# Kernel optimization log

Hardware: AMD Instinct MI355X
Metric: run time of the kernel (lower is better)

## Reference

```python
import jax, jax.numpy as jnp
import numpy as np
import math

B, N, DIM = 16, 1024, 384
DEPTH, HEADS, DH = 6, 6, 64
INNER = HEADS * DH          # 384
MLP = 1536
LN_EPS = 1e-5


def setup_inputs() -> dict:
    key = jax.random.key(0)
    ks = jax.random.split(key, 7)
    s = 0.02
    x = jax.random.normal(ks[0], (B, N, DIM), dtype=jnp.float32)
    ln1_g = jnp.ones((DEPTH, DIM), jnp.float32)
    ln1_b = jnp.zeros((DEPTH, DIM), jnp.float32)
    qkv_w = jax.random.normal(ks[1], (DEPTH, DIM, 3 * INNER), jnp.float32) * s
    temp = jnp.full((DEPTH,), math.log(DH ** -0.5), jnp.float32)
    out_w = jax.random.normal(ks[2], (DEPTH, INNER, DIM), jnp.float32) * s
    out_b = jnp.zeros((DEPTH, DIM), jnp.float32)
    ln2_g = jnp.ones((DEPTH, DIM), jnp.float32)
    ln2_b = jnp.zeros((DEPTH, DIM), jnp.float32)
    ff_w1 = jax.random.normal(ks[3], (DEPTH, DIM, MLP), jnp.float32) * s
    ff_b1 = jnp.zeros((DEPTH, MLP), jnp.float32)
    ff_w2 = jax.random.normal(ks[4], (DEPTH, MLP, DIM), jnp.float32) * s
    ff_b2 = jnp.zeros((DEPTH, DIM), jnp.float32)
    return dict(x=x, ln1_g=ln1_g, ln1_b=ln1_b, qkv_w=qkv_w, temp=temp,
                out_w=out_w, out_b=out_b, ln2_g=ln2_g, ln2_b=ln2_b,
                ff_w1=ff_w1, ff_b1=ff_b1, ff_w2=ff_w2, ff_b2=ff_b2)


def _ln(x, g, b):
    m = jnp.mean(x, axis=-1, keepdims=True)
    v = jnp.var(x, axis=-1, keepdims=True)
    return (x - m) * jax.lax.rsqrt(v + LN_EPS) * g + b


def reference(x, ln1_g, ln1_b, qkv_w, temp, out_w, out_b,
              ln2_g, ln2_b, ff_w1, ff_b1, ff_w2, ff_b2):
    neg = -jnp.finfo(x.dtype).max
    eye = jnp.eye(N, dtype=bool)

    def step(x, p):
        g1, b1, wqkv, t, wo, bo, g2, b2, w1, bb1, w2, bb2 = p
        # --- PreNorm + LSA attention ---
        h = _ln(x, g1, b1)
        qkv = h @ wqkv                              # [B, N, 3*INNER]
        q, k, v = jnp.split(qkv, 3, axis=-1)
        split_heads = lambda a: a.reshape(B, N, HEADS, DH).transpose(0, 2, 1, 3)
        q, k, v = split_heads(q), split_heads(k), split_heads(v)
        dots = jnp.einsum('bhnd,bhmd->bhnm', q, k) * jnp.exp(t)
        dots = jnp.where(eye, neg, dots)            # mask diagonal (LSA)
        attn = jax.nn.softmax(dots, axis=-1)
        o = jnp.einsum('bhnm,bhmd->bhnd', attn, v)
        o = o.transpose(0, 2, 1, 3).reshape(B, N, INNER)
        x = x + o @ wo + bo
        # --- PreNorm + FeedForward (exact GELU) ---
        h2 = _ln(x, g2, b2)
        ff = jax.nn.gelu(h2 @ w1 + bb1, approximate=False) @ w2 + bb2
        x = x + ff
        return x, None

    params = (ln1_g, ln1_b, qkv_w, temp, out_w, out_b,
              ln2_g, ln2_b, ff_w1, ff_b1, ff_w2, ff_b2)
    x, _ = jax.lax.scan(step, x, params)
    return x
```

## Files before the change

### kernel.cpp

```cpp
#include <hip/hip_runtime.h>
#include <hip/hip_bf16.h>
#include <math.h>

#define B_     16
#define NTOK   1024
#define DIM_   384
#define DEPTH_ 6
#define HEADS_ 6
#define DH_    64
#define MLP_   1536
#define MTOT   (B_ * NTOK)
#define NBH    (B_ * HEADS_)
#define QKV_PLANE ((size_t)NBH * NTOK * DH_)

typedef unsigned short u16;
typedef unsigned int u32;
typedef short short8 __attribute__((ext_vector_type(8)));
typedef float f32x4 __attribute__((ext_vector_type(4)));

static __device__ __forceinline__ u16 f2b(float f) {
    __hip_bfloat16 h = __float2bfloat16(f);
    return *reinterpret_cast<u16*>(&h);
}

#define GLOAD_LDS16(gp, lp)                                                     \
    __builtin_amdgcn_global_load_lds(                                           \
        (const __attribute__((address_space(1))) void*)(gp),                    \
        (__attribute__((address_space(3))) void*)(lp), 16, 0, 0)

#define WAIT_VM(N)                                                              \
    do { asm volatile("s_waitcnt vmcnt(" #N ")" ::: "memory");                  \
         __builtin_amdgcn_sched_barrier(0); } while (0)
#define WAIT_LGKM0()                                                            \
    do { asm volatile("s_waitcnt lgkmcnt(0)" ::: "memory");                     \
         __builtin_amdgcn_sched_barrier(0); } while (0)

__launch_bounds__(256)
__global__ void transpose_w_kernel(const float* __restrict__ W, u16* __restrict__ WT,
                                   int K, int N) {
    const int layer = blockIdx.z;
    W  += (size_t)layer * K * N;
    WT += (size_t)layer * K * N;
    __shared__ u16 tile[64 * 72];
    const int t = threadIdx.x;
    const int k0 = blockIdx.x * 64, n0 = blockIdx.y * 64;
    const int row = t >> 2, cs = (t & 3) * 16;
    const float4* src = reinterpret_cast<const float4*>(W + (size_t)(k0 + row) * N + n0 + cs);
#pragma unroll
    for (int i = 0; i < 4; i++) {
        float4 f = src[i];
        tile[row * 72 + cs + i * 4 + 0] = f2b(f.x);
        tile[row * 72 + cs + i * 4 + 1] = f2b(f.y);
        tile[row * 72 + cs + i * 4 + 2] = f2b(f.z);
        tile[row * 72 + cs + i * 4 + 3] = f2b(f.w);
    }
    __syncthreads();
    const int nrow = row, ks = cs;
    u16 vals[16] __attribute__((aligned(16)));
#pragma unroll
    for (int e = 0; e < 16; e++) vals[e] = tile[(ks + e) * 72 + nrow];
    u16* dst = WT + (size_t)(n0 + nrow) * K + k0 + ks;
    *reinterpret_cast<short8*>(dst)     = *reinterpret_cast<short8*>(&vals[0]);
    *reinterpret_cast<short8*>(dst + 8) = *reinterpret_cast<short8*>(&vals[8]);
}

__launch_bounds__(256)
__global__ void ln_kernel(const float* __restrict__ x, const float* __restrict__ g,
                          const float* __restrict__ b, u16* __restrict__ h) {
    const int tok  = blockIdx.x * 4 + (threadIdx.x >> 6);
    const int lane = threadIdx.x & 63;
    const float* xr = x + (size_t)tok * DIM_;
    float v[6];
    float s = 0.f;
#pragma unroll
    for (int i = 0; i < 6; i++) { v[i] = xr[lane + i * 64]; s += v[i]; }
#pragma unroll
    for (int m = 1; m < 64; m <<= 1) s += __shfl_xor(s, m);
    const float mean = s * (1.f / 384.f);
    float qs = 0.f;
#pragma unroll
    for (int i = 0; i < 6; i++) { float d = v[i] - mean; qs += d * d; }
#pragma unroll
    for (int m = 1; m < 64; m <<= 1) qs += __shfl_xor(qs, m);
    const float inv = rsqrtf(qs * (1.f / 384.f) + 1e-5f);
    u16* hr = h + (size_t)tok * DIM_;
#pragma unroll
    for (int i = 0; i < 6; i++) {
        const int c = lane + i * 64;
        hr[c] = f2b((v[i] - mean) * inv * g[c] + b[c]);
    }
}

enum { EPI_QKV = 0, EPI_RES = 1, EPI_GELU = 2 };

template <int EPI>
__launch_bounds__(256)
__global__ void gemm_kernel(const u16* __restrict__ A, const u16* __restrict__ BT, int K,
                            const float* __restrict__ bias, const float* __restrict__ resid,
                            float* __restrict__ outf, u16* __restrict__ outb, int ldc,
                            u16* __restrict__ qkv_base) {
    __shared__ u16 As[3][4096];
    __shared__ u16 Bs[3][4096];
    const int t = threadIdx.x;
    const int lane = t & 63, w = t >> 6;
    const int wm = w >> 1, wn = w & 1;
    const int m0 = blockIdx.x * 128, n0 = blockIdx.y * 128;

    f32x4 acc[4][4] = {};

    const int c0p = w * 1024, c1p = w * 1024 + 512;
    const int seg = (lane & 3) * 8;
    const u16* agp0 = A  + (size_t)(m0 + (w * 2 + 0) * 16 + (lane >> 2)) * K + seg;
    const u16* agp1 = A  + (size_t)(m0 + (w * 2 + 1) * 16 + (lane >> 2)) * K + seg;
    const u16* bgp0 = BT + (size_t)(n0 + (w * 2 + 0) * 16 + (lane >> 2)) * K + seg;
    const u16* bgp1 = BT + (size_t)(n0 + (w * 2 + 1) * 16 + (lane >> 2)) * K + seg;

    const int T = K >> 5;
    GLOAD_LDS16(agp0,      &As[0][c0p]);
    GLOAD_LDS16(agp1,      &As[0][c1p]);
    GLOAD_LDS16(bgp0,      &Bs[0][c0p]);
    GLOAD_LDS16(bgp1,      &Bs[0][c1p]);
    GLOAD_LDS16(agp0 + 32, &As[1][c0p]);
    GLOAD_LDS16(agp1 + 32, &As[1][c1p]);
    GLOAD_LDS16(bgp0 + 32, &Bs[1][c0p]);
    GLOAD_LDS16(bgp1 + 32, &Bs[1][c1p]);

    int b0 = 0, b1 = 1, b2 = 2;
    for (int tt = 0; tt < T; ++tt) {
        if (tt + 2 < T) {
            const int kk = (tt + 2) << 5;
            GLOAD_LDS16(agp0 + kk, &As[b2][c0p]);
            GLOAD_LDS16(agp1 + kk, &As[b2][c1p]);
            GLOAD_LDS16(bgp0 + kk, &Bs[b2][c0p]);
            GLOAD_LDS16(bgp1 + kk, &Bs[b2][c1p]);
            WAIT_VM(8);
        } else if (tt + 1 < T) {
            WAIT_VM(4);
        } else {
            WAIT_VM(0);
        }
        __builtin_amdgcn_s_barrier();
        short8 af[4], bf[4];
#pragma unroll
        for (int i = 0; i < 4; i++)
            af[i] = *reinterpret_cast<const short8*>(
                &As[b0][(wm * 64 + i * 16 + (lane & 15)) * 32 + (lane >> 4) * 8]);
#pragma unroll
        for (int j = 0; j < 4; j++)
            bf[j] = *reinterpret_cast<const short8*>(
                &Bs[b0][(wn * 64 + j * 16 + (lane & 15)) * 32 + (lane >> 4) * 8]);
#pragma unroll
        for (int i = 0; i < 4; i++)
#pragma unroll
            for (int j = 0; j < 4; j++)
                acc[i][j] = __builtin_amdgcn_mfma_f32_16x16x32_bf16(af[i], bf[j], acc[i][j], 0, 0, 0);
        WAIT_LGKM0();
        __builtin_amdgcn_s_barrier();
        const int tmp = b0; b0 = b1; b1 = b2; b2 = tmp;
    }

    const int rbase = (lane >> 4) * 4;
    const int cb = lane & 15;
#pragma unroll
    for (int i = 0; i < 4; i++) {
#pragma unroll
        for (int j = 0; j < 4; j++) {
            if constexpr (EPI == EPI_QKV) {
                const int c = n0 + wn * 64 + j * 16 + cb;
                const int which = c / 384;
                const int cc = c - which * 384;
                const int head = cc >> 6, dh = cc & 63;
                const int nb = m0 + wm * 64 + i * 16 + rbase;
                const int b = nb >> 10, nt = nb & 1023;
                const size_t bh = (size_t)(b * HEADS_ + head);
                if (which == 2) {
                    u16 pk[4] __attribute__((aligned(8)));
#pragma unroll
                    for (int r = 0; r < 4; r++) pk[r] = f2b(acc[i][j][r]);
                    const int nsw = (nt & ~63) | ((((nt >> 3) & 7) ^ (dh & 7)) << 3) | (nt & 7);
                    *reinterpret_cast<uint2*>(
                        &qkv_base[2 * QKV_PLANE + bh * 65536 + (size_t)dh * 1024 + nsw]) =
                        *reinterpret_cast<uint2*>(pk);
                } else if (which == 1) {
#pragma unroll
                    for (int r = 0; r < 4; r++) {
                        const int n = nt + r;
                        const int dsw = (((dh >> 3) ^ (n & 7)) << 3) | (dh & 7);
                        qkv_base[QKV_PLANE + bh * 65536 + (size_t)n * 64 + dsw] =
                            f2b(acc[i][j][r]);
                    }
                } else {
#pragma unroll
                    for (int r = 0; r < 4; r++)
                        qkv_base[bh * 65536 + (size_t)(nt + r) * 64 + dh] = f2b(acc[i][j][r]);
                }
            } else {
#pragma unroll
                for (int r = 0; r < 4; r++) {
                    const int m = m0 + wm * 64 + i * 16 + rbase + r;
                    const int c = n0 + wn * 64 + j * 16 + cb;
                    const float val = acc[i][j][r];
                    if constexpr (EPI == EPI_RES) {
                        outf[(size_t)m * ldc + c] = resid[(size_t)m * ldc + c] + bias[c] + val;
                    } else {
                        const float xg = val + bias[c];
                        const float ge = 0.5f * xg * (1.0f + erff(xg * 0.70710678118f));
                        outb[(size_t)m * ldc + c] = f2b(ge);
                    }
                }
            }
        }
    }
}

__launch_bounds__(256)
__global__ void attn_kernel(const u16* __restrict__ q, const u16* __restrict__ k,
                            const u16* __restrict__ v, const float* __restrict__ temp,
                            u16* __restrict__ o) {
    __shared__ u16 Kt[2][4096];
    __shared__ u16 Vt[2][4096];
    __shared__ u16 Ps[4][16 * 80];
    const int t = threadIdx.x, lane = t & 63, w = t >> 6;
    const int g8 = lane >> 4, qi = lane & 15;
    const int bh = blockIdx.x, q0 = blockIdx.y * 64;
    const float scale2 = __expf(temp[0]) * 1.4426950408889634f;
    const size_t base = (size_t)bh * (NTOK * DH_);

    short8 bq[2];
#pragma unroll
    for (int s = 0; s < 2; s++)
        bq[s] = *reinterpret_cast<const short8*>(
            &q[base + (size_t)(q0 + w * 16 + qi) * 64 + s * 32 + g8 * 8]);

    float m_s = -3.0e38f, l_s = 0.f;
    f32x4 accO[4] = {};
    const int qglob = q0 + w * 16 + qi;

    const int srow = w * 8 + (lane >> 3);
    const int schunk = (lane & 7) * 8;
    const u16* kg0 = k + base + (size_t)srow * 64 + schunk;
    const u16* vg0 = v + base + (size_t)srow * 1024 + schunk;
    const int wp = w * 512;

    GLOAD_LDS16(kg0,             &Kt[0][wp]);
    GLOAD_LDS16(kg0 + 32 * 64,   &Kt[0][wp + 2048]);
    GLOAD_LDS16(vg0,             &Vt[0][wp]);
    GLOAD_LDS16(vg0 + 32 * 1024, &Vt[0][wp + 2048]);

    int cur = 0;
    for (int jt = 0; jt < 16; ++jt) {
        if (jt + 1 < 16) {
            const size_t jn = (size_t)(jt + 1) * 64;
            GLOAD_LDS16(kg0 + jn * 64,            &Kt[cur ^ 1][wp]);
            GLOAD_LDS16(kg0 + jn * 64 + 32 * 64,  &Kt[cur ^ 1][wp + 2048]);
            GLOAD_LDS16(vg0 + jn,                 &Vt[cur ^ 1][wp]);
            GLOAD_LDS16(vg0 + jn + 32 * 1024,     &Vt[cur ^ 1][wp + 2048]);
            WAIT_VM(4);
        } else {
            WAIT_VM(0);
        }
        __builtin_amdgcn_s_barrier();

        f32x4 sf[4] = {};
#pragma unroll
        for (int c = 0; c < 4; c++) {
            const int krow = c * 16 + qi;
#pragma unroll
            for (int s = 0; s < 2; s++) {
                short8 af = *reinterpret_cast<const short8*>(
                    &Kt[cur][krow * 64 + (((s * 4 + g8) ^ (krow & 7)) << 3)]);
                sf[c] = __builtin_amdgcn_mfma_f32_16x16x32_bf16(af, bq[s], sf[c], 0, 0, 0);
            }
        }

        float p[4][4];
        float vmax = -3.0e38f;
        if (jt * 64 == q0) {
#pragma unroll
            for (int c = 0; c < 4; c++)
#pragma unroll
                for (int r = 0; r < 4; r++) {
                    float sv = sf[c][r] * scale2;
                    if (jt * 64 + c * 16 + g8 * 4 + r == qglob) sv = -3.0e37f;
                    p[c][r] = sv;
                    vmax = fmaxf(vmax, sv);
                }
        } else {
#pragma unroll
            for (int c = 0; c < 4; c++)
#pragma unroll
                for (int r = 0; r < 4; r++) {
                    const float sv = sf[c][r] * scale2;
                    p[c][r] = sv;
                    vmax = fmaxf(vmax, sv);
                }
        }
        vmax = fmaxf(vmax, __shfl_xor(vmax, 16));
        vmax = fmaxf(vmax, __shfl_xor(vmax, 32));

        if (!__all(vmax - m_s <= 11.0f)) {
            const float mnew = fmaxf(m_s, vmax);
            const float alpha = exp2f(m_s - mnew);
            m_s = mnew;
            l_s *= alpha;
#pragma unroll
            for (int r = 0; r < 4; r++) {
                const float a_r = __shfl(alpha, g8 * 4 + r, 64);
#pragma unroll
                for (int g = 0; g < 4; g++) accO[g][r] *= a_r;
            }
        }

        float tsum = 0.f;
#pragma unroll
        for (int c = 0; c < 4; c++)
#pragma unroll
            for (int r = 0; r < 4; r++) {
                const float pe = exp2f(p[c][r] - m_s);
                p[c][r] = pe;
                tsum += pe;
            }
        tsum += __shfl_xor(tsum, 16);
        tsum += __shfl_xor(tsum, 32);
        l_s += tsum;

#pragma unroll
        for (int c = 0; c < 4; c++) {
            u32 lo = (u32)f2b(p[c][0]) | ((u32)f2b(p[c][1]) << 16);
            u32 hi = (u32)f2b(p[c][2]) | ((u32)f2b(p[c][3]) << 16);
            uint2 pr; pr.x = lo; pr.y = hi;
            *reinterpret_cast<uint2*>(&Ps[w][qi * 80 + c * 16 + g8 * 4]) = pr;
        }

#pragma unroll
        for (int s = 0; s < 2; s++) {
            short8 ap = *reinterpret_cast<const short8*>(&Ps[w][qi * 80 + s * 32 + g8 * 8]);
#pragma unroll
            for (int g = 0; g < 4; g++) {
                const int vrow = g * 16 + qi;
                short8 bv = *reinterpret_cast<const short8*>(
                    &Vt[cur][vrow * 64 + (((s * 4 + g8) ^ (vrow & 7)) << 3)]);
                accO[g] = __builtin_amdgcn_mfma_f32_16x16x32_bf16(ap, bv, accO[g], 0, 0, 0);
            }
        }
        WAIT_LGKM0();
        __builtin_amdgcn_s_barrier();
        cur ^= 1;
    }

    const int bidx = bh / HEADS_, head = bh % HEADS_;
#pragma unroll
    for (int r = 0; r < 4; r++) {
        const float li = __shfl(l_s, g8 * 4 + r, 64);
        const float linv = 1.f / li;
        const int n = q0 + w * 16 + g8 * 4 + r;
#pragma unroll
        for (int g = 0; g < 4; g++) {
            const int dh = g * 16 + qi;
            o[((size_t)(bidx * NTOK + n)) * DIM_ + head * DH_ + dh] = f2b(accO[g][r] * linv);
        }
    }
}

extern "C" void kernel_launch(void* const* d_in, const int* in_sizes, int n_in,
                              void* d_out, int out_size, void* d_ws, size_t ws_size,
                              hipStream_t stream) {
    const float* x_in  = (const float*)d_in[0];
    const float* ln1_g = (const float*)d_in[1];
    const float* ln1_b = (const float*)d_in[2];
    const float* qkv_w = (const float*)d_in[3];
    const float* temp  = (const float*)d_in[4];
    const float* out_w = (const float*)d_in[5];
    const float* out_b = (const float*)d_in[6];
    const float* ln2_g = (const float*)d_in[7];
    const float* ln2_b = (const float*)d_in[8];
    const float* ff_w1 = (const float*)d_in[9];
    const float* ff_b1 = (const float*)d_in[10];
    const float* ff_w2 = (const float*)d_in[11];
    const float* ff_b2 = (const float*)d_in[12];

    char* ws = (char*)d_ws;
    size_t off = 0;
    auto alloc = [&](size_t bytes) -> void* {
        void* p = ws + off;
        off += (bytes + 255) & ~(size_t)255;
        return p;
    };
    u16* wt_qkv = (u16*)alloc((size_t)DEPTH_ * 1152 * 384 * 2);
    u16* wt_out = (u16*)alloc((size_t)DEPTH_ * 384 * 384 * 2);
    u16* wt_ff1 = (u16*)alloc((size_t)DEPTH_ * 1536 * 384 * 2);
    u16* wt_ff2 = (u16*)alloc((size_t)DEPTH_ * 384 * 1536 * 2);
    u16* H      = (u16*)alloc((size_t)MTOT * DIM_ * 2);
    u16* QKV    = (u16*)alloc((size_t)MTOT * MLP_ * 2);
    u16* MID    = QKV;

    float* X = (float*)d_out;

    hipMemcpyAsync(X, x_in, (size_t)MTOT * DIM_ * sizeof(float),
                   hipMemcpyDeviceToDevice, stream);

    transpose_w_kernel<<<dim3(6, 18, DEPTH_), 256, 0, stream>>>(qkv_w, wt_qkv, 384, 1152);
    transpose_w_kernel<<<dim3(6, 6, DEPTH_), 256, 0, stream>>>(out_w, wt_out, 384, 384);
    transpose_w_kernel<<<dim3(6, 24, DEPTH_), 256, 0, stream>>>(ff_w1, wt_ff1, 384, 1536);
    transpose_w_kernel<<<dim3(24, 6, DEPTH_), 256, 0, stream>>>(ff_w2, wt_ff2, 1536, 384);

    for (int layer = 0; layer < DEPTH_; layer++) {
        ln_kernel<<<4096, 256, 0, stream>>>(X, ln1_g + layer * DIM_, ln1_b + layer * DIM_, H);
        gemm_kernel<EPI_QKV><<<dim3(128, 9), 256, 0, stream>>>(
            H, wt_qkv + (size_t)layer * 1152 * 384, 384,
            nullptr, nullptr, nullptr, nullptr, 0, QKV);
        attn_kernel<<<dim3(96, 16), 256, 0, stream>>>(
            QKV, QKV + QKV_PLANE, QKV + 2 * QKV_PLANE, temp + layer, H);
        gemm_kernel<EPI_RES><<<dim3(128, 3), 256, 0, stream>>>(
            H, wt_out + (size_t)layer * 384 * 384, 384,
            out_b + layer * DIM_, X, X, nullptr, DIM_, nullptr);
        ln_kernel<<<4096, 256, 0, stream>>>(X, ln2_g + layer * DIM_, ln2_b + layer * DIM_, H);
        gemm_kernel<EPI_GELU><<<dim3(128, 12), 256, 0, stream>>>(
            H, wt_ff1 + (size_t)layer * 1536 * 384, 384,
            ff_b1 + layer * MLP_, nullptr, nullptr, MID, MLP_, nullptr);
        gemm_kernel<EPI_RES><<<dim3(128, 3), 256, 0, stream>>>(
            MID, wt_ff2 + (size_t)layer * 384 * 1536, 1536,
            ff_b2 + layer * DIM_, X, X, nullptr, DIM_, nullptr);
    }
}
```

Baseline: 1.371 ms.

## Process two 16-row query tiles per wave in attention to reuse K/V loads

```diff
diff --git a/kernel.cpp b/kernel.cpp
--- a/kernel.cpp
+++ b/kernel.cpp
@@ -219,22 +219,27 @@
                             u16* __restrict__ o) {
     __shared__ u16 Kt[2][4096];
     __shared__ u16 Vt[2][4096];
-    __shared__ u16 Ps[4][16 * 80];
+    __shared__ u16 Ps[4][32 * 80];
     const int t = threadIdx.x, lane = t & 63, w = t >> 6;
     const int g8 = lane >> 4, qi = lane & 15;
-    const int bh = blockIdx.x, q0 = blockIdx.y * 64;
+    const int bh = blockIdx.x, q0 = blockIdx.y * 128;
     const float scale2 = __expf(temp[0]) * 1.4426950408889634f;
     const size_t base = (size_t)bh * (NTOK * DH_);
 
-    short8 bq[2];
-#pragma unroll
-    for (int s = 0; s < 2; s++)
-        bq[s] = *reinterpret_cast<const short8*>(
-            &q[base + (size_t)(q0 + w * 16 + qi) * 64 + s * 32 + g8 * 8]);
-
-    float m_s = -3.0e38f, l_s = 0.f;
-    f32x4 accO[4] = {};
-    const int qglob = q0 + w * 16 + qi;
+    short8 bq0[2], bq1[2];
+#pragma unroll
+    for (int s = 0; s < 2; s++) {
+        bq0[s] = *reinterpret_cast<const short8*>(
+            &q[base + (size_t)(q0 + w * 32 + qi) * 64 + s * 32 + g8 * 8]);
+        bq1[s] = *reinterpret_cast<const short8*>(
+            &q[base + (size_t)(q0 + w * 32 + 16 + qi) * 64 + s * 32 + g8 * 8]);
+    }
+
+    float m0 = -3.0e38f, l0 = 0.f, m1 = -3.0e38f, l1 = 0.f;
+    f32x4 accO0[4] = {}, accO1[4] = {};
+    const int qg0 = q0 + w * 32 + qi;
+    const int qg1 = qg0 + 16;
+    const int diag_jt = (q0 >> 6) + (w >> 1);
 
     const int srow = w * 8 + (lane >> 3);
     const int schunk = (lane & 7) * 8;
@@ -261,7 +266,8 @@
         }
         __builtin_amdgcn_s_barrier();
 
-        f32x4 sf[4] = {};
+        f32x4 sf0[4] = {}, sf1[4] = {};
+        __builtin_amdgcn_s_setprio(1);
 #pragma unroll
         for (int c = 0; c < 4; c++) {
             const int krow = c * 16 + qi;
@@ -269,80 +275,109 @@
             for (int s = 0; s < 2; s++) {
                 short8 af = *reinterpret_cast<const short8*>(
                     &Kt[cur][krow * 64 + (((s * 4 + g8) ^ (krow & 7)) << 3)]);
-                sf[c] = __builtin_amdgcn_mfma_f32_16x16x32_bf16(af, bq[s], sf[c], 0, 0, 0);
-            }
-        }
-
-        float p[4][4];
-        float vmax = -3.0e38f;
-        if (jt * 64 == q0) {
+                sf0[c] = __builtin_amdgcn_mfma_f32_16x16x32_bf16(af, bq0[s], sf0[c], 0, 0, 0);
+                sf1[c] = __builtin_amdgcn_mfma_f32_16x16x32_bf16(af, bq1[s], sf1[c], 0, 0, 0);
+            }
+        }
+        __builtin_amdgcn_s_setprio(0);
+
+        if (jt == diag_jt) {
 #pragma unroll
             for (int c = 0; c < 4; c++)
 #pragma unroll
                 for (int r = 0; r < 4; r++) {
-                    float sv = sf[c][r] * scale2;
-                    if (jt * 64 + c * 16 + g8 * 4 + r == qglob) sv = -3.0e37f;
-                    p[c][r] = sv;
-                    vmax = fmaxf(vmax, sv);
+                    const int kvg = jt * 64 + c * 16 + g8 * 4 + r;
+                    if (kvg == qg0) sf0[c][r] = -1.0e30f;
+                    if (kvg == qg1) sf1[c][r] = -1.0e30f;
                 }
-        } else {
+        }
+
+        float vmax0 = -3.0e38f, vmax1 = -3.0e38f;
+#pragma unroll
+        for (int c = 0; c < 4; c++)
+#pragma unroll
+            for (int r = 0; r < 4; r++) {
+                vmax0 = fmaxf(vmax0, sf0[c][r]);
+                vmax1 = fmaxf(vmax1, sf1[c][r]);
+            }
+        vmax0 = fmaxf(vmax0, __shfl_xor(vmax0, 16));
+        vmax0 = fmaxf(vmax0, __shfl_xor(vmax0, 32));
+        vmax1 = fmaxf(vmax1, __shfl_xor(vmax1, 16));
+        vmax1 = fmaxf(vmax1, __shfl_xor(vmax1, 32));
+        const float smax0 = vmax0 * scale2;
+        const float smax1 = vmax1 * scale2;
+
+        if (!__all((smax0 - m0 <= 11.0f) && (smax1 - m1 <= 11.0f))) {
+            const float nm0 = fmaxf(m0, smax0), nm1 = fmaxf(m1, smax1);
+            const float al0 = exp2f(m0 - nm0), al1 = exp2f(m1 - nm1);
+            m0 = nm0; m1 = nm1; l0 *= al0; l1 *= al1;
+#pragma unroll
+            for (int r = 0; r < 4; r++) {
+                const float a0 = __shfl(al0, g8 * 4 + r, 64);
+                const float a1 = __shfl(al1, g8 * 4 + r, 64);
+#pragma unroll
+                for (int g = 0; g < 4; g++) { accO0[g][r] *= a0; accO1[g][r] *= a1; }
+            }
+        }
+
+        {
+            float pe[4][4];
+            float ts = 0.f;
 #pragma unroll
             for (int c = 0; c < 4; c++)
 #pragma unroll
                 for (int r = 0; r < 4; r++) {
-                    const float sv = sf[c][r] * scale2;
-                    p[c][r] = sv;
-                    vmax = fmaxf(vmax, sv);
+                    const float e = exp2f(fmaf(sf0[c][r], scale2, -m0));
+                    pe[c][r] = e; ts += e;
                 }
-        }
-        vmax = fmaxf(vmax, __shfl_xor(vmax, 16));
-        vmax = fmaxf(vmax, __shfl_xor(vmax, 32));
-
-        if (!__all(vmax - m_s <= 11.0f)) {
-            const float mnew = fmaxf(m_s, vmax);
-            const float alpha = exp2f(m_s - mnew);
-            m_s = mnew;
-            l_s *= alpha;
-#pragma unroll
-            for (int r = 0; r < 4; r++) {
-                const float a_r = __shfl(alpha, g8 * 4 + r, 64);
-#pragma unroll
-                for (int g = 0; g < 4; g++) accO[g][r] *= a_r;
-            }
-        }
-
-        float tsum = 0.f;
-#pragma unroll
-        for (int c = 0; c < 4; c++)
-#pragma unroll
-            for (int r = 0; r < 4; r++) {
-                const float pe = exp2f(p[c][r] - m_s);
-                p[c][r] = pe;
-                tsum += pe;
-            }
-        tsum += __shfl_xor(tsum, 16);
-        tsum += __shfl_xor(tsum, 32);
-        l_s += tsum;
-
-#pragma unroll
-        for (int c = 0; c < 4; c++) {
-            u32 lo = (u32)f2b(p[c][0]) | ((u32)f2b(p[c][1]) << 16);
-            u32 hi = (u32)f2b(p[c][2]) | ((u32)f2b(p[c][3]) << 16);
-            uint2 pr; pr.x = lo; pr.y = hi;
-            *reinterpret_cast<uint2*>(&Ps[w][qi * 80 + c * 16 + g8 * 4]) = pr;
-        }
-
+            ts += __shfl_xor(ts, 16);
+            ts += __shfl_xor(ts, 32);
+            l0 += ts;
+#pragma unroll
+            for (int c = 0; c < 4; c++) {
+                u32 lo = (u32)f2b(pe[c][0]) | ((u32)f2b(pe[c][1]) << 16);
+                u32 hi = (u32)f2b(pe[c][2]) | ((u32)f2b(pe[c][3]) << 16);
+                uint2 pr; pr.x = lo; pr.y = hi;
+                *reinterpret_cast<uint2*>(&Ps[w][qi * 80 + c * 16 + g8 * 4]) = pr;
+            }
+        }
+        {
+            float pe[4][4];
+            float ts = 0.f;
+#pragma unroll
+            for (int c = 0; c < 4; c++)
+#pragma unroll
+                for (int r = 0; r < 4; r++) {
+                    const float e = exp2f(fmaf(sf1[c][r], scale2, -m1));
+                    pe[c][r] = e; ts += e;
+                }
+            ts += __shfl_xor(ts, 16);
+            ts += __shfl_xor(ts, 32);
+            l1 += ts;
+#pragma unroll
+            for (int c = 0; c < 4; c++) {
+                u32 lo = (u32)f2b(pe[c][0]) | ((u32)f2b(pe[c][1]) << 16);
+                u32 hi = (u32)f2b(pe[c][2]) | ((u32)f2b(pe[c][3]) << 16);
+                uint2 pr; pr.x = lo; pr.y = hi;
+                *reinterpret_cast<uint2*>(&Ps[w][(16 + qi) * 80 + c * 16 + g8 * 4]) = pr;
+            }
+        }
+
+        __builtin_amdgcn_s_setprio(1);
 #pragma unroll
         for (int s = 0; s < 2; s++) {
-            short8 ap = *reinterpret_cast<const short8*>(&Ps[w][qi * 80 + s * 32 + g8 * 8]);
+            short8 ap0 = *reinterpret_cast<const short8*>(&Ps[w][qi * 80 + s * 32 + g8 * 8]);
+            short8 ap1 = *reinterpret_cast<const short8*>(&Ps[w][(16 + qi) * 80 + s * 32 + g8 * 8]);
 #pragma unroll
             for (int g = 0; g < 4; g++) {
                 const int vrow = g * 16 + qi;
                 short8 bv = *reinterpret_cast<const short8*>(
                     &Vt[cur][vrow * 64 + (((s * 4 + g8) ^ (vrow & 7)) << 3)]);
-                accO[g] = __builtin_amdgcn_mfma_f32_16x16x32_bf16(ap, bv, accO[g], 0, 0, 0);
-            }
-        }
+                accO0[g] = __builtin_amdgcn_mfma_f32_16x16x32_bf16(ap0, bv, accO0[g], 0, 0, 0);
+                accO1[g] = __builtin_amdgcn_mfma_f32_16x16x32_bf16(ap1, bv, accO1[g], 0, 0, 0);
+            }
+        }
+        __builtin_amdgcn_s_setprio(0);
         WAIT_LGKM0();
         __builtin_amdgcn_s_barrier();
         cur ^= 1;
@@ -351,13 +386,16 @@
     const int bidx = bh / HEADS_, head = bh % HEADS_;
 #pragma unroll
     for (int r = 0; r < 4; r++) {
-        const float li = __shfl(l_s, g8 * 4 + r, 64);
-        const float linv = 1.f / li;
-        const int n = q0 + w * 16 + g8 * 4 + r;
+        const float li0 = __shfl(l0, g8 * 4 + r, 64);
+        const float li1 = __shfl(l1, g8 * 4 + r, 64);
+        const float inv0 = 1.f / li0;
+        const float inv1 = 1.f / li1;
+        const int n = q0 + w * 32 + g8 * 4 + r;
 #pragma unroll
         for (int g = 0; g < 4; g++) {
             const int dh = g * 16 + qi;
-            o[((size_t)(bidx * NTOK + n)) * DIM_ + head * DH_ + dh] = f2b(accO[g][r] * linv);
+            o[((size_t)(bidx * NTOK + n)) * DIM_ + head * DH_ + dh]      = f2b(accO0[g][r] * inv0);
+            o[((size_t)(bidx * NTOK + n + 16)) * DIM_ + head * DH_ + dh] = f2b(accO1[g][r] * inv1);
         }
     }
 }
@@ -409,7 +447,7 @@
         gemm_kernel<EPI_QKV><<<dim3(128, 9), 256, 0, stream>>>(
             H, wt_qkv + (size_t)layer * 1152 * 384, 384,
             nullptr, nullptr, nullptr, nullptr, 0, QKV);
-        attn_kernel<<<dim3(96, 16), 256, 0, stream>>>(
+        attn_kernel<<<dim3(96, 8), 256, 0, stream>>>(
             QKV, QKV + QKV_PLANE, QKV + 2 * QKV_PLANE, temp + layer, H);
         gemm_kernel<EPI_RES><<<dim3(128, 3), 256, 0, stream>>>(
             H, wt_out + (size_t)layer * 384 * 384, 384,
```

Measured after the change: 1.389 ms. Within noise of the previous version (+1.3%).
